# Optimization experiments

Measured on AMD Instinct MI355X. Metric: run time of the kernel, lower is better.

The kernel has to match this reference:

```python
import jax, jax.numpy as jnp
import numpy as np
import math

# ---- model dimensions (match init_kwargs / input_specs) ----
B, LQ, LK = 2, 1024, 1024          # batch, q_dim (query seq len), kv_dim (key seq len)
D_HEAD, H = 64, 16                 # head_size = d_model // n_heads, n_heads
D_MODEL = D_HEAD * H               # 1024
C_FACTOR = 5
U_SEL  = int(C_FACTOR * math.log(LQ))   # u  = 34 selected (top) queries
U_SAMP = int(LQ * math.log(LK))         # U  = 7097 randomly sampled keys


def setup_inputs() -> dict:
    key = jax.random.key(0)
    kq, kk, kv, kw, kb = jax.random.split(key, 5)
    q = jax.random.normal(kq, (B, LQ, D_HEAD), dtype=jnp.float32)
    k = jax.random.normal(kk, (B, LK, D_HEAD), dtype=jnp.float32)
    v = jax.random.normal(kv, (B, LK, D_HEAD), dtype=jnp.float32)
    # final projection Linear(n_heads*head_size, d_model), stored as (in, out)
    W_proj = jax.random.normal(kw, (D_MODEL, D_MODEL), dtype=jnp.float32) * 0.02
    b_proj = jax.random.normal(kb, (D_MODEL,), dtype=jnp.float32) * 0.02
    return {"q": q, "k": k, "v": v, "W_proj": W_proj, "b_proj": b_proj}


def _probsparse_head(head_key, q, k, v):
    """One ProbSparse head: q,k,v are (B, L, D_HEAD). Returns (B, LQ, D_HEAD)."""
    b_idx = jnp.arange(B)[:, None]
    # _sampler: per-batch random key indices, shape (B, U_SAMP)
    idx = jax.random.randint(head_key, (B, U_SAMP), 0, LK)
    k_bar = k[b_idx, idx]                                   # (B, U_SAMP, D)
    # sparsity measure M = max - mean over sampled scores
    s_bar = jnp.einsum('bqd,bud->bqu', q, k_bar)            # (B, LQ, U_SAMP)
    M = s_bar.max(axis=-1) - s_bar.mean(axis=-1)            # (B, LQ)
    _, top_idx = jax.lax.top_k(M, U_SEL)                    # (B, U_SEL)
    q_bar = q[b_idx, top_idx]                               # (B, U_SEL, D)
    # attention on the selected queries only; scale = sqrt(kv seq len) as in source
    attn = jnp.einsum('bud,bkd->buk', q_bar, k) / jnp.sqrt(jnp.float32(LK))
    attn = jax.nn.softmax(attn, axis=-1)
    s1 = jnp.einsum('buk,bkd->bud', attn, v)                # (B, U_SEL, D)
    # non-selected rows get mean(v); selected rows get attention output
    s = jnp.broadcast_to(v.mean(axis=1, keepdims=True), (B, LQ, D_HEAD))
    return s.at[b_idx, top_idx].set(s1)


def reference(q, k, v, W_proj, b_proj):
    # heads share q,k,v; differ only in random key sampling -> map sequentially over head keys
    head_keys = jax.random.split(jax.random.key(42), H)
    heads = jax.lax.map(lambda hk: _probsparse_head(hk, q, k, v), head_keys)  # (H,B,LQ,D)
    # concat along feature dim == transpose + reshape
    attn_out = jnp.transpose(heads, (1, 2, 0, 3)).reshape(B, LQ, H * D_HEAD)
    return attn_out @ W_proj + b_proj                        # (B, LQ, D_MODEL)
```

## Files before the change

kernel.cpp:

```cpp
#include <hip/hip_runtime.h>
#include <math.h>
#include <stdint.h>
#include <stddef.h>


#define BB     2
#define LQ     1024
#define LK     1024
#define DH     64
#define NH     16
#define DM     1024
#define USEL   34
#define USAMP  7097
#define NSLICE 8
#define NJ     8
#define JS     (LK / NJ)

#define THREEFRY_PARTITIONABLE 1

__device__ __forceinline__ uint32_t rotl32(uint32_t x, int d) {
  return (x << d) | (x >> (32 - d));
}

__device__ __forceinline__ void threefry2x32(uint32_t k0, uint32_t k1,
                                             uint32_t x0, uint32_t x1,
                                             uint32_t& o0, uint32_t& o1) {
  uint32_t ks2 = k0 ^ k1 ^ 0x1BD11BDAu;
  x0 += k0; x1 += k1;
#define TFR(r) { x0 += x1; x1 = rotl32(x1, (r)); x1 ^= x0; }
  TFR(13) TFR(15) TFR(26) TFR(6)
  x0 += k1; x1 += ks2 + 1u;
  TFR(17) TFR(29) TFR(16) TFR(24)
  x0 += ks2; x1 += k0 + 2u;
  TFR(13) TFR(15) TFR(26) TFR(6)
  x0 += k0; x1 += k1 + 3u;
  TFR(17) TFR(29) TFR(16) TFR(24)
  x0 += k1; x1 += ks2 + 4u;
  TFR(13) TFR(15) TFR(26) TFR(6)
  x0 += ks2; x1 += k0 + 5u;
#undef TFR
  o0 = x0; o1 = x1;
}

__global__ __launch_bounds__(1024) void k_sample(unsigned* __restrict__ counts) {
  int hb = blockIdx.x, h = hb >> 1, b = hb & 1;
  int t = threadIdx.x;
  __shared__ unsigned hist[LK];
  hist[t] = 0u;
  uint32_t sk0, sk1;
#if THREEFRY_PARTITIONABLE
  {
    uint32_t hk0, hk1;
    threefry2x32(0u, 42u, 0u, (uint32_t)h, hk0, hk1);
    threefry2x32(hk0, hk1, 0u, 1u, sk0, sk1);
  }
#else
  {
    uint32_t hk0, hk1, a0, a1, b0_, b1_, c0_, c1_;
    int i0 = 2 * h, i1 = 2 * h + 1;
    if (i0 < 16) { threefry2x32(0u, 42u, (uint32_t)i0, (uint32_t)(i0 + 16), a0, a1); hk0 = a0; }
    else         { threefry2x32(0u, 42u, (uint32_t)(i0 - 16), (uint32_t)i0, a0, a1); hk0 = a1; }
    if (i1 < 16) { threefry2x32(0u, 42u, (uint32_t)i1, (uint32_t)(i1 + 16), a0, a1); hk1 = a0; }
    else         { threefry2x32(0u, 42u, (uint32_t)(i1 - 16), (uint32_t)i1, a0, a1); hk1 = a1; }
    threefry2x32(hk0, hk1, 0u, 2u, b0_, b1_);
    threefry2x32(hk0, hk1, 1u, 3u, c0_, c1_);
    sk0 = b1_; sk1 = c1_;
  }
#endif
  __syncthreads();
  for (int j = t; j < USAMP; j += 1024) {
    uint32_t o0, o1, bits;
#if THREEFRY_PARTITIONABLE
    threefry2x32(sk0, sk1, 0u, (uint32_t)(b * USAMP + j), o0, o1);
    bits = o0 ^ o1;
#else
    threefry2x32(sk0, sk1, (uint32_t)j, (uint32_t)(j + USAMP), o0, o1);
    bits = (b == 0) ? o0 : o1;
#endif
    atomicAdd(&hist[bits & (LK - 1)], 1u);
  }
  __syncthreads();
  counts[(size_t)hb * LK + t] = hist[t];
}

__global__ __launch_bounds__(256) void k_means(const float* __restrict__ kk,
                                               const float* __restrict__ v,
                                               const unsigned* __restrict__ counts,
                                               float* __restrict__ kmean_part,
                                               float* __restrict__ vmean_part) {
  int task = blockIdx.y, s = blockIdx.x, t = threadIdx.x;
  int d4 = t & 15, jsub = t >> 4;
  __shared__ float4 part[16][16];
  float4 acc = make_float4(0.f, 0.f, 0.f, 0.f);
  if (task < NH * BB) {
    int b = task & 1;
    const unsigned* cnt = counts + (size_t)task * LK;
    const float4* kb4 = (const float4*)(kk + (size_t)b * LK * DH);
#pragma unroll
    for (int jj = 0; jj < LK / (16 * NSLICE); jj++) {
      int j = s * (LK / NSLICE) + jsub + 16 * jj;
      float c = (float)cnt[j];
      float4 kv = kb4[j * 16 + d4];
      acc.x += c * kv.x; acc.y += c * kv.y; acc.z += c * kv.z; acc.w += c * kv.w;
    }
  } else {
    int b = task - NH * BB;
    const float4* vb4 = (const float4*)(v + (size_t)b * LK * DH);
#pragma unroll
    for (int jj = 0; jj < LK / (16 * NSLICE); jj++) {
      int j = s * (LK / NSLICE) + jsub + 16 * jj;
      float4 kv = vb4[j * 16 + d4];
      acc.x += kv.x; acc.y += kv.y; acc.z += kv.z; acc.w += kv.w;
    }
  }
  part[jsub][d4] = acc;
  __syncthreads();
  if (t < 16) {
    float4 sum = part[0][t];
#pragma unroll
    for (int x = 1; x < 16; x++) {
      float4 p = part[x][t];
      sum.x += p.x; sum.y += p.y; sum.z += p.z; sum.w += p.w;
    }
    if (task < NH * BB) {
      float* dst = kmean_part + ((size_t)s * NH * BB + task) * DH;
      const float sc = 1.0f / (float)USAMP;
      dst[t * 4 + 0] = sum.x * sc; dst[t * 4 + 1] = sum.y * sc;
      dst[t * 4 + 2] = sum.z * sc; dst[t * 4 + 3] = sum.w * sc;
    } else {
      float* dst = vmean_part + ((size_t)s * BB + (task - NH * BB)) * DH;
      const float sc = 1.0f / (float)LK;
      dst[t * 4 + 0] = sum.x * sc; dst[t * 4 + 1] = sum.y * sc;
      dst[t * 4 + 2] = sum.z * sc; dst[t * 4 + 3] = sum.w * sc;
    }
  }
}

__global__ __launch_bounds__(256) void k_scores(const float* __restrict__ q,
                                                const float* __restrict__ k,
                                                float* __restrict__ S) {
  __shared__ float Qt[DH][68];
  __shared__ float Kt[DH][68];
  int b = blockIdx.z;
  int i0 = blockIdx.y * 64, j0 = blockIdx.x * 64;
  int t = threadIdx.x;
  const float* qb = q + ((size_t)b * LQ + i0) * DH;
  const float* kb = k + ((size_t)b * LK + j0) * DH;
#pragma unroll
  for (int rep = 0; rep < 4; rep++) {
    int lin = (rep * 256 + t) * 4;
    int r = lin >> 6, c = lin & 63;
    float4 qv = *(const float4*)(qb + (size_t)r * DH + c);
    float4 kv = *(const float4*)(kb + (size_t)r * DH + c);
    Qt[c][r] = qv.x; Qt[c + 1][r] = qv.y; Qt[c + 2][r] = qv.z; Qt[c + 3][r] = qv.w;
    Kt[c][r] = kv.x; Kt[c + 1][r] = kv.y; Kt[c + 2][r] = kv.z; Kt[c + 3][r] = kv.w;
  }
  __syncthreads();
  int tx = t & 15, ty = t >> 4;
  float acc[4][4] = {};
#pragma unroll 8
  for (int d = 0; d < DH; d++) {
    float4 av = *(const float4*)&Qt[d][ty * 4];
    float4 bv = *(const float4*)&Kt[d][tx * 4];
    acc[0][0] += av.x * bv.x; acc[0][1] += av.x * bv.y; acc[0][2] += av.x * bv.z; acc[0][3] += av.x * bv.w;
    acc[1][0] += av.y * bv.x; acc[1][1] += av.y * bv.y; acc[1][2] += av.y * bv.z; acc[1][3] += av.y * bv.w;
    acc[2][0] += av.z * bv.x; acc[2][1] += av.z * bv.y; acc[2][2] += av.z * bv.z; acc[2][3] += av.z * bv.w;
    acc[3][0] += av.w * bv.x; acc[3][1] += av.w * bv.y; acc[3][2] += av.w * bv.z; acc[3][3] += av.w * bv.w;
  }
  float* Sb = S + ((size_t)b * LQ + i0) * LK + j0;
#pragma unroll
  for (int r = 0; r < 4; r++) {
    *(float4*)(Sb + (size_t)(ty * 4 + r) * LK + tx * 4) =
        make_float4(acc[r][0], acc[r][1], acc[r][2], acc[r][3]);
  }
}

__global__ __launch_bounds__(256) void k_M(const float* __restrict__ q,
                                           const float* __restrict__ S,
                                           const unsigned* __restrict__ counts,
                                           const float* __restrict__ kmean_part,
                                           float* __restrict__ M) {
  int b = blockIdx.y;
  __shared__ uint32_t mask[NH][LK / 32];
  __shared__ float kmean_s[NH][DH];
  int t = threadIdx.x;
  for (int w = t; w < NH * (LK / 32); w += 256) {
    int h = w >> 5, blk = w & 31;
    const unsigned* cnt = counts + ((size_t)h * BB + b) * LK + blk * 32;
    uint32_t m = 0;
    for (int z = 0; z < 32; z++) m |= (cnt[z] != 0u ? 1u : 0u) << z;
    mask[h][blk] = m;
  }
  for (int idx = t; idx < NH * DH; idx += 256) {
    int h = idx >> 6, d = idx & 63;
    float sum = 0.f;
#pragma unroll
    for (int sl = 0; sl < NSLICE; sl++)
      sum += kmean_part[((size_t)sl * NH * BB + h * BB + b) * DH + d];
    kmean_s[h][d] = sum;
  }
  __syncthreads();
  int lane = t & 63, w4 = t >> 6;
  int i = blockIdx.x * 4 + w4;
  const float* Srow = S + ((size_t)b * LQ + i) * LK;
  float mx[NH];
#pragma unroll
  for (int h = 0; h < NH; h++) mx[h] = -INFINITY;
  for (int j = lane; j < LK; j += 64) {
    float s = Srow[j];
#pragma unroll
    for (int h = 0; h < NH; h++) {
      bool on = (mask[h][j >> 5] >> (j & 31)) & 1u;
      mx[h] = fmaxf(mx[h], on ? s : -INFINITY);
    }
  }
#pragma unroll
  for (int h = 0; h < NH; h++) {
#pragma unroll
    for (int off = 32; off > 0; off >>= 1) mx[h] = fmaxf(mx[h], __shfl_xor(mx[h], off));
  }
  float qv = q[((size_t)b * LQ + i) * DH + lane];
#pragma unroll
  for (int h = 0; h < NH; h++) {
    float p = qv * kmean_s[h][lane];
#pragma unroll
    for (int off = 32; off > 0; off >>= 1) p += __shfl_xor(p, off);
    mx[h] -= p;
  }
  if (lane == 0) {
#pragma unroll
    for (int h = 0; h < NH; h++) M[((size_t)h * BB + b) * LQ + i] = mx[h];
  }
}

__global__ __launch_bounds__(256) void k_topk(const float* __restrict__ M,
                                              int* __restrict__ topidx) {
  int hb = blockIdx.x, t = threadIdx.x;
  __shared__ float vals[LQ];
  __shared__ float wv[4];
  __shared__ int   wi[4];
  for (int i = t; i < LQ; i += 256) vals[i] = M[(size_t)hb * LQ + i];
  __syncthreads();
  int lane = t & 63, w = t >> 6;
  for (int u = 0; u < USEL; u++) {
    float bv = -INFINITY; int bi = 0x7fffffff;
#pragma unroll
    for (int r = 0; r < 4; r++) {
      int i = r * 256 + t;
      float x = vals[i];
      if (x > bv) { bv = x; bi = i; }
    }
#pragma unroll
    for (int off = 32; off > 0; off >>= 1) {
      float ov = __shfl_xor(bv, off);
      int   oi = __shfl_xor(bi, off);
      if (ov > bv || (ov == bv && oi < bi)) { bv = ov; bi = oi; }
    }
    if (lane == 0) { wv[w] = bv; wi[w] = bi; }
    __syncthreads();
    if (t == 0) {
      float fv = wv[0]; int fi = wi[0];
#pragma unroll
      for (int x = 1; x < 4; x++)
        if (wv[x] > fv || (wv[x] == fv && wi[x] < fi)) { fv = wv[x]; fi = wi[x]; }
      topidx[hb * USEL + u] = fi;
      vals[fi] = -INFINITY;
    }
    __syncthreads();
  }
}

__global__ __launch_bounds__(256) void k_pv(const float* __restrict__ S,
                                            const float* __restrict__ v,
                                            const int* __restrict__ topidx,
                                            float* __restrict__ delta_part,
                                            float* __restrict__ ssum_part) {
  int hb = blockIdx.y, s = blockIdx.x, b = hb & 1;
  int t = threadIdx.x, d = t & 63, g = t >> 6;
  __shared__ float p[USEL][JS];
  __shared__ float part[4][USEL][DH];
  for (int idx = t; idx < USEL * JS; idx += 256) {
    int u = idx >> 7, jj = idx & (JS - 1);
    int i = topidx[hb * USEL + u];
    float xs = S[((size_t)b * LQ + i) * LK + s * JS + jj];
    p[u][jj] = expf(xs * 0.03125f);
  }
  __syncthreads();
  float vreg[32];
  const float* vb = v + ((size_t)b * LK + s * JS + g * 32) * DH + d;
#pragma unroll
  for (int jj = 0; jj < 32; jj++) vreg[jj] = vb[(size_t)jj * DH];
  for (int u = 0; u < USEL; u++) {
    float acc = 0.f;
#pragma unroll
    for (int j4 = 0; j4 < 8; j4++) {
      float4 pp = *(const float4*)&p[u][g * 32 + j4 * 4];
      acc += pp.x * vreg[j4 * 4] + pp.y * vreg[j4 * 4 + 1] +
             pp.z * vreg[j4 * 4 + 2] + pp.w * vreg[j4 * 4 + 3];
    }
    part[g][u][d] = acc;
  }
  if (t < USEL * 4) {
    int u = t >> 2, ch = t & 3;
    float sum = 0.f;
#pragma unroll
    for (int jj = 0; jj < 32; jj++) sum += p[u][ch * 32 + jj];
    ssum_part[(((size_t)s * NH * BB + hb) * USEL + u) * 4 + ch] = sum;
  }
  __syncthreads();
  for (int idx = t; idx < USEL * DH; idx += 256) {
    int u = idx >> 6, dd = idx & 63;
    float sum = part[0][u][dd] + part[1][u][dd] + part[2][u][dd] + part[3][u][dd];
    delta_part[(((size_t)s * NH * BB + hb) * USEL + u) * DH + dd] = sum;
  }
}

__global__ __launch_bounds__(256) void k_base(const float* __restrict__ W,
                                              const float* __restrict__ vmean_part,
                                              float* __restrict__ base_part) {
  __shared__ float vm[DH];
  int b = blockIdx.y, hc = blockIdx.z;
  int o = blockIdx.x * 256 + threadIdx.x;
  if (threadIdx.x < DH) {
    float s = 0.f;
#pragma unroll
    for (int sl = 0; sl < NSLICE; sl++)
      s += vmean_part[((size_t)sl * BB + b) * DH + threadIdx.x];
    vm[threadIdx.x] = s;
  }
  __syncthreads();
  const float* Wr = W + (size_t)hc * DH * DM + o;
  float acc = 0.f;
#pragma unroll
  for (int d = 0; d < DH; d++) acc += vm[d] * Wr[(size_t)d * DM];
  base_part[((size_t)hc * BB + b) * DM + o] = acc;
}

__global__ __launch_bounds__(256) void k_fill(const float* __restrict__ base_part,
                                              const float* __restrict__ bproj,
                                              float* __restrict__ out) {
  int idx = blockIdx.x * 256 + threadIdx.x;
  int o4 = idx & (DM / 4 - 1);
  int b = (idx >> 18) & 1;
  float4 bs = ((const float4*)bproj)[o4];
#pragma unroll
  for (int hc = 0; hc < NH; hc++) {
    float4 p = ((const float4*)base_part)[((size_t)hc * BB + b) * (DM / 4) + o4];
    bs.x += p.x; bs.y += p.y; bs.z += p.z; bs.w += p.w;
  }
  ((float4*)out)[idx] = bs;
}

__global__ __launch_bounds__(256) void k_corr(const float* __restrict__ W,
                                              const int* __restrict__ topidx,
                                              const float* __restrict__ delta_part,
                                              const float* __restrict__ ssum_part,
                                              const float* __restrict__ vmean_part,
                                              float* __restrict__ out) {
  int u = blockIdx.x, hb = blockIdx.y;
  int h = hb >> 1, b = hb & 1;
  int t = threadIdx.x;
  __shared__ float dl[DH];
  int i = topidx[hb * USEL + u];
  if (t < DH) {
    float ss = 0.f, dr = 0.f, vm = 0.f;
#pragma unroll
    for (int sl = 0; sl < NJ; sl++) {
      const float* sp = ssum_part + (((size_t)sl * NH * BB + hb) * USEL + u) * 4;
      ss += sp[0] + sp[1] + sp[2] + sp[3];
      dr += delta_part[(((size_t)sl * NH * BB + hb) * USEL + u) * DH + t];
    }
#pragma unroll
    for (int sl = 0; sl < NSLICE; sl++)
      vm += vmean_part[((size_t)sl * BB + b) * DH + t];
    dl[t] = dr / ss - vm;
  }
  __syncthreads();
  const float* Wh = W + (size_t)h * DH * DM;
  float* orow = out + ((size_t)b * LQ + i) * DM;
#pragma unroll
  for (int rep = 0; rep < 4; rep++) {
    int o = rep * 256 + t;
    float acc = 0.f;
#pragma unroll 16
    for (int d = 0; d < DH; d++) acc += dl[d] * Wh[(size_t)d * DM + o];
    atomicAdd(&orow[o], acc);
  }
}

extern "C" void kernel_launch(void* const* d_in, const int* in_sizes, int n_in,
                              void* d_out, int out_size, void* d_ws, size_t ws_size,
                              hipStream_t stream) {
  const float* q  = (const float*)d_in[0];
  const float* k  = (const float*)d_in[1];
  const float* v  = (const float*)d_in[2];
  const float* W  = (const float*)d_in[3];
  const float* bp = (const float*)d_in[4];
  float* out = (float*)d_out;

  float* S = out;

  char* w = (char*)d_ws;
  unsigned* counts     = (unsigned*)w;  w += (size_t)NH * BB * LK * 4;
  float*    kmean_part = (float*)w;     w += (size_t)NSLICE * NH * BB * DH * 4;
  float*    vmean_part = (float*)w;     w += (size_t)NSLICE * BB * DH * 4;
  float*    base_part  = (float*)w;     w += (size_t)NH * BB * DM * 4;
  float*    delta_part = (float*)w;     w += (size_t)NJ * NH * BB * USEL * DH * 4;
  float*    ssum_part  = (float*)w;     w += (size_t)NJ * NH * BB * USEL * 4 * 4;
  float*    M          = (float*)w;     w += (size_t)NH * BB * LQ * 4;
  int*      topidx     = (int*)w;       w += (size_t)NH * BB * USEL * 4;
  if ((size_t)(w - (char*)d_ws) > ws_size) return;

  k_sample<<<NH * BB, 1024, 0, stream>>>(counts);
  k_means <<<dim3(NSLICE, NH * BB + BB), 256, 0, stream>>>(k, v, counts, kmean_part, vmean_part);
  k_scores<<<dim3(LK / 64, LQ / 64, BB), 256, 0, stream>>>(q, k, S);
  k_M     <<<dim3(LQ / 4, BB), 256, 0, stream>>>(q, S, counts, kmean_part, M);
  k_topk  <<<NH * BB, 256, 0, stream>>>(M, topidx);
  k_pv    <<<dim3(NJ, NH * BB), 256, 0, stream>>>(S, v, topidx, delta_part, ssum_part);
  k_base  <<<dim3(DM / 256, BB, NH), 256, 0, stream>>>(W, vmean_part, base_part);
  k_fill  <<<(BB * LQ * DM / 4) / 256, 256, 0, stream>>>(base_part, bp, out);
  k_corr  <<<dim3(USEL, NH * BB), 256, 0, stream>>>(W, topidx, delta_part, ssum_part, vmean_part, out);
}
```

Baseline: 178.2 us.

## Merge independent kernels into heterogeneous launches and move scores buffer to workspace

Combines the sampling, mean, and score kernels into one launch with block-index dispatch, fuses the M computation with the base projection, and fuses top-k with the output fill, cutting nine launches to five. Sampling now builds the key bitmask and full key means in one block per head, so the partial-slice reductions disappear. The score matrix moves from the output buffer to workspace, which the fused fill requires because it now runs before k_pv reads S. The trade-off is uneven block workloads within each launch, and the 32 sampling blocks do serial work while the GEMM blocks run.

```diff
diff --git a/kernel.cpp b/kernel.cpp
--- a/kernel.cpp
+++ b/kernel.cpp
@@ -12,9 +12,11 @@
 #define DM     1024
 #define USEL   34
 #define USAMP  7097
-#define NSLICE 8
 #define NJ     8
 #define JS     (LK / NJ)
+#define NSC    512
+#define NMB    512
+#define NTK    32
 
 #define THREEFRY_PARTITIONABLE 1
 
@@ -42,231 +44,266 @@
   o0 = x0; o1 = x1;
 }
 
-__global__ __launch_bounds__(1024) void k_sample(unsigned* __restrict__ counts) {
-  int hb = blockIdx.x, h = hb >> 1, b = hb & 1;
-  int t = threadIdx.x;
-  __shared__ unsigned hist[LK];
-  hist[t] = 0u;
-  uint32_t sk0, sk1;
+__device__ __forceinline__ void randint_key(int h, uint32_t& sk0, uint32_t& sk1) {
 #if THREEFRY_PARTITIONABLE
-  {
-    uint32_t hk0, hk1;
-    threefry2x32(0u, 42u, 0u, (uint32_t)h, hk0, hk1);
-    threefry2x32(hk0, hk1, 0u, 1u, sk0, sk1);
-  }
+  uint32_t hk0, hk1;
+  threefry2x32(0u, 42u, 0u, (uint32_t)h, hk0, hk1);
+  threefry2x32(hk0, hk1, 0u, 1u, sk0, sk1);
 #else
-  {
-    uint32_t hk0, hk1, a0, a1, b0_, b1_, c0_, c1_;
-    int i0 = 2 * h, i1 = 2 * h + 1;
-    if (i0 < 16) { threefry2x32(0u, 42u, (uint32_t)i0, (uint32_t)(i0 + 16), a0, a1); hk0 = a0; }
-    else         { threefry2x32(0u, 42u, (uint32_t)(i0 - 16), (uint32_t)i0, a0, a1); hk0 = a1; }
-    if (i1 < 16) { threefry2x32(0u, 42u, (uint32_t)i1, (uint32_t)(i1 + 16), a0, a1); hk1 = a0; }
-    else         { threefry2x32(0u, 42u, (uint32_t)(i1 - 16), (uint32_t)i1, a0, a1); hk1 = a1; }
-    threefry2x32(hk0, hk1, 0u, 2u, b0_, b1_);
-    threefry2x32(hk0, hk1, 1u, 3u, c0_, c1_);
-    sk0 = b1_; sk1 = c1_;
-  }
+  uint32_t hk0, hk1, a0, a1, b0_, b1_, c0_, c1_;
+  int i0 = 2 * h, i1 = 2 * h + 1;
+  if (i0 < 16) { threefry2x32(0u, 42u, (uint32_t)i0, (uint32_t)(i0 + 16), a0, a1); hk0 = a0; }
+  else         { threefry2x32(0u, 42u, (uint32_t)(i0 - 16), (uint32_t)i0, a0, a1); hk0 = a1; }
+  if (i1 < 16) { threefry2x32(0u, 42u, (uint32_t)i1, (uint32_t)(i1 + 16), a0, a1); hk1 = a0; }
+  else         { threefry2x32(0u, 42u, (uint32_t)(i1 - 16), (uint32_t)i1, a0, a1); hk1 = a1; }
+  threefry2x32(hk0, hk1, 0u, 2u, b0_, b1_);
+  threefry2x32(hk0, hk1, 1u, 3u, c0_, c1_);
+  sk0 = b1_; sk1 = c1_;
 #endif
-  __syncthreads();
-  for (int j = t; j < USAMP; j += 1024) {
-    uint32_t o0, o1, bits;
+}
+
+__global__ __launch_bounds__(256) void k_prep_scores(const float* __restrict__ q,
+                                                     const float* __restrict__ kk,
+                                                     const float* __restrict__ v,
+                                                     float* __restrict__ S,
+                                                     unsigned* __restrict__ mask_g,
+                                                     float* __restrict__ kmean,
+                                                     float* __restrict__ vmean) {
+  __shared__ __align__(16) char smem[34816];
+  int bx = blockIdx.x, t = threadIdx.x;
+  if (bx < NSC) {
+    float (*Qt)[68] = (float (*)[68])smem;
+    float (*Kt)[68] = (float (*)[68])(smem + 17408);
+    int b = bx >> 8, it = (bx >> 4) & 15, jt = bx & 15;
+    int i0 = it * 64, j0 = jt * 64;
+    const float* qb = q + ((size_t)b * LQ + i0) * DH;
+    const float* kb = kk + ((size_t)b * LK + j0) * DH;
+#pragma unroll
+    for (int rep = 0; rep < 4; rep++) {
+      int lin = (rep * 256 + t) * 4;
+      int r = lin >> 6, c = lin & 63;
+      float4 qv = *(const float4*)(qb + (size_t)r * DH + c);
+      float4 kv = *(const float4*)(kb + (size_t)r * DH + c);
+      Qt[c][r] = qv.x; Qt[c + 1][r] = qv.y; Qt[c + 2][r] = qv.z; Qt[c + 3][r] = qv.w;
+      Kt[c][r] = kv.x; Kt[c + 1][r] = kv.y; Kt[c + 2][r] = kv.z; Kt[c + 3][r] = kv.w;
+    }
+    __syncthreads();
+    int tx = t & 15, ty = t >> 4;
+    float acc[4][4] = {};
+#pragma unroll 8
+    for (int d = 0; d < DH; d++) {
+      float4 av = *(const float4*)&Qt[d][ty * 4];
+      float4 bv = *(const float4*)&Kt[d][tx * 4];
+      acc[0][0] += av.x * bv.x; acc[0][1] += av.x * bv.y; acc[0][2] += av.x * bv.z; acc[0][3] += av.x * bv.w;
+      acc[1][0] += av.y * bv.x; acc[1][1] += av.y * bv.y; acc[1][2] += av.y * bv.z; acc[1][3] += av.y * bv.w;
+      acc[2][0] += av.z * bv.x; acc[2][1] += av.z * bv.y; acc[2][2] += av.z * bv.z; acc[2][3] += av.z * bv.w;
+      acc[3][0] += av.w * bv.x; acc[3][1] += av.w * bv.y; acc[3][2] += av.w * bv.z; acc[3][3] += av.w * bv.w;
+    }
+    float* Sb = S + ((size_t)b * LQ + i0) * LK + j0;
+#pragma unroll
+    for (int r = 0; r < 4; r++) {
+      *(float4*)(Sb + (size_t)(ty * 4 + r) * LK + tx * 4) =
+          make_float4(acc[r][0], acc[r][1], acc[r][2], acc[r][3]);
+    }
+  } else if (bx < NSC + NH * BB) {
+    int hb = bx - NSC, h = hb >> 1, b = hb & 1;
+    unsigned* hist = (unsigned*)smem;
+    float4 (*part)[16] = (float4 (*)[16])(smem + 4096);
+    hist[t] = 0u; hist[t + 256] = 0u; hist[t + 512] = 0u; hist[t + 768] = 0u;
+    uint32_t sk0, sk1;
+    randint_key(h, sk0, sk1);
+    __syncthreads();
+    for (int j = t; j < USAMP; j += 256) {
+      uint32_t o0, o1, bits;
 #if THREEFRY_PARTITIONABLE
-    threefry2x32(sk0, sk1, 0u, (uint32_t)(b * USAMP + j), o0, o1);
-    bits = o0 ^ o1;
+      threefry2x32(sk0, sk1, 0u, (uint32_t)(b * USAMP + j), o0, o1);
+      bits = o0 ^ o1;
 #else
-    threefry2x32(sk0, sk1, (uint32_t)j, (uint32_t)(j + USAMP), o0, o1);
-    bits = (b == 0) ? o0 : o1;
+      threefry2x32(sk0, sk1, (uint32_t)j, (uint32_t)(j + USAMP), o0, o1);
+      bits = (b == 0) ? o0 : o1;
 #endif
-    atomicAdd(&hist[bits & (LK - 1)], 1u);
-  }
-  __syncthreads();
-  counts[(size_t)hb * LK + t] = hist[t];
-}
-
-__global__ __launch_bounds__(256) void k_means(const float* __restrict__ kk,
-                                               const float* __restrict__ v,
-                                               const unsigned* __restrict__ counts,
-                                               float* __restrict__ kmean_part,
-                                               float* __restrict__ vmean_part) {
-  int task = blockIdx.y, s = blockIdx.x, t = threadIdx.x;
-  int d4 = t & 15, jsub = t >> 4;
-  __shared__ float4 part[16][16];
-  float4 acc = make_float4(0.f, 0.f, 0.f, 0.f);
-  if (task < NH * BB) {
-    int b = task & 1;
-    const unsigned* cnt = counts + (size_t)task * LK;
+      atomicAdd(&hist[bits & (LK - 1)], 1u);
+    }
+    __syncthreads();
+    if (t < LK / 32) {
+      uint32_t m = 0;
+      for (int z = 0; z < 32; z++) m |= (hist[t * 32 + z] != 0u ? 1u : 0u) << z;
+      mask_g[hb * (LK / 32) + t] = m;
+    }
+    int d4 = t & 15, jsub = t >> 4;
     const float4* kb4 = (const float4*)(kk + (size_t)b * LK * DH);
-#pragma unroll
-    for (int jj = 0; jj < LK / (16 * NSLICE); jj++) {
-      int j = s * (LK / NSLICE) + jsub + 16 * jj;
-      float c = (float)cnt[j];
+    float4 acc = make_float4(0.f, 0.f, 0.f, 0.f);
+#pragma unroll 8
+    for (int jj = 0; jj < LK / 16; jj++) {
+      int j = jsub + 16 * jj;
+      float c = (float)hist[j];
       float4 kv = kb4[j * 16 + d4];
       acc.x += c * kv.x; acc.y += c * kv.y; acc.z += c * kv.z; acc.w += c * kv.w;
     }
+    part[jsub][d4] = acc;
+    __syncthreads();
+    if (t < 16) {
+      float4 sum = part[0][t];
+#pragma unroll
+      for (int x = 1; x < 16; x++) {
+        float4 p = part[x][t];
+        sum.x += p.x; sum.y += p.y; sum.z += p.z; sum.w += p.w;
+      }
+      const float sc = 1.0f / (float)USAMP;
+      float* dst = kmean + (size_t)hb * DH;
+      dst[t * 4 + 0] = sum.x * sc; dst[t * 4 + 1] = sum.y * sc;
+      dst[t * 4 + 2] = sum.z * sc; dst[t * 4 + 3] = sum.w * sc;
+    }
   } else {
-    int b = task - NH * BB;
+    int b = bx - NSC - NH * BB;
+    float4 (*part)[16] = (float4 (*)[16])smem;
+    int d4 = t & 15, jsub = t >> 4;
     const float4* vb4 = (const float4*)(v + (size_t)b * LK * DH);
-#pragma unroll
-    for (int jj = 0; jj < LK / (16 * NSLICE); jj++) {
-      int j = s * (LK / NSLICE) + jsub + 16 * jj;
+    float4 acc = make_float4(0.f, 0.f, 0.f, 0.f);
+#pragma unroll 8
+    for (int jj = 0; jj < LK / 16; jj++) {
+      int j = jsub + 16 * jj;
       float4 kv = vb4[j * 16 + d4];
       acc.x += kv.x; acc.y += kv.y; acc.z += kv.z; acc.w += kv.w;
     }
-  }
-  part[jsub][d4] = acc;
-  __syncthreads();
-  if (t < 16) {
-    float4 sum = part[0][t];
-#pragma unroll
-    for (int x = 1; x < 16; x++) {
-      float4 p = part[x][t];
-      sum.x += p.x; sum.y += p.y; sum.z += p.z; sum.w += p.w;
-    }
-    if (task < NH * BB) {
-      float* dst = kmean_part + ((size_t)s * NH * BB + task) * DH;
-      const float sc = 1.0f / (float)USAMP;
+    part[jsub][d4] = acc;
+    __syncthreads();
+    if (t < 16) {
+      float4 sum = part[0][t];
+#pragma unroll
+      for (int x = 1; x < 16; x++) {
+        float4 p = part[x][t];
+        sum.x += p.x; sum.y += p.y; sum.z += p.z; sum.w += p.w;
+      }
+      const float sc = 1.0f / (float)LK;
+      float* dst = vmean + (size_t)b * DH;
       dst[t * 4 + 0] = sum.x * sc; dst[t * 4 + 1] = sum.y * sc;
       dst[t * 4 + 2] = sum.z * sc; dst[t * 4 + 3] = sum.w * sc;
-    } else {
-      float* dst = vmean_part + ((size_t)s * BB + (task - NH * BB)) * DH;
-      const float sc = 1.0f / (float)LK;
-      dst[t * 4 + 0] = sum.x * sc; dst[t * 4 + 1] = sum.y * sc;
-      dst[t * 4 + 2] = sum.z * sc; dst[t * 4 + 3] = sum.w * sc;
-    }
-  }
-}
-
-__global__ __launch_bounds__(256) void k_scores(const float* __restrict__ q,
-                                                const float* __restrict__ k,
-                                                float* __restrict__ S) {
-  __shared__ float Qt[DH][68];
-  __shared__ float Kt[DH][68];
-  int b = blockIdx.z;
-  int i0 = blockIdx.y * 64, j0 = blockIdx.x * 64;
-  int t = threadIdx.x;
-  const float* qb = q + ((size_t)b * LQ + i0) * DH;
-  const float* kb = k + ((size_t)b * LK + j0) * DH;
-#pragma unroll
-  for (int rep = 0; rep < 4; rep++) {
-    int lin = (rep * 256 + t) * 4;
-    int r = lin >> 6, c = lin & 63;
-    float4 qv = *(const float4*)(qb + (size_t)r * DH + c);
-    float4 kv = *(const float4*)(kb + (size_t)r * DH + c);
-    Qt[c][r] = qv.x; Qt[c + 1][r] = qv.y; Qt[c + 2][r] = qv.z; Qt[c + 3][r] = qv.w;
-    Kt[c][r] = kv.x; Kt[c + 1][r] = kv.y; Kt[c + 2][r] = kv.z; Kt[c + 3][r] = kv.w;
-  }
-  __syncthreads();
-  int tx = t & 15, ty = t >> 4;
-  float acc[4][4] = {};
-#pragma unroll 8
-  for (int d = 0; d < DH; d++) {
-    float4 av = *(const float4*)&Qt[d][ty * 4];
-    float4 bv = *(const float4*)&Kt[d][tx * 4];
-    acc[0][0] += av.x * bv.x; acc[0][1] += av.x * bv.y; acc[0][2] += av.x * bv.z; acc[0][3] += av.x * bv.w;
-    acc[1][0] += av.y * bv.x; acc[1][1] += av.y * bv.y; acc[1][2] += av.y * bv.z; acc[1][3] += av.y * bv.w;
-    acc[2][0] += av.z * bv.x; acc[2][1] += av.z * bv.y; acc[2][2] += av.z * bv.z; acc[2][3] += av.z * bv.w;
-    acc[3][0] += av.w * bv.x; acc[3][1] += av.w * bv.y; acc[3][2] += av.w * bv.z; acc[3][3] += av.w * bv.w;
-  }
-  float* Sb = S + ((size_t)b * LQ + i0) * LK + j0;
-#pragma unroll
-  for (int r = 0; r < 4; r++) {
-    *(float4*)(Sb + (size_t)(ty * 4 + r) * LK + tx * 4) =
-        make_float4(acc[r][0], acc[r][1], acc[r][2], acc[r][3]);
-  }
-}
-
-__global__ __launch_bounds__(256) void k_M(const float* __restrict__ q,
-                                           const float* __restrict__ S,
-                                           const unsigned* __restrict__ counts,
-                                           const float* __restrict__ kmean_part,
-                                           float* __restrict__ M) {
-  int b = blockIdx.y;
-  __shared__ uint32_t mask[NH][LK / 32];
-  __shared__ float kmean_s[NH][DH];
-  int t = threadIdx.x;
-  for (int w = t; w < NH * (LK / 32); w += 256) {
-    int h = w >> 5, blk = w & 31;
-    const unsigned* cnt = counts + ((size_t)h * BB + b) * LK + blk * 32;
-    uint32_t m = 0;
-    for (int z = 0; z < 32; z++) m |= (cnt[z] != 0u ? 1u : 0u) << z;
-    mask[h][blk] = m;
-  }
-  for (int idx = t; idx < NH * DH; idx += 256) {
-    int h = idx >> 6, d = idx & 63;
-    float sum = 0.f;
-#pragma unroll
-    for (int sl = 0; sl < NSLICE; sl++)
-      sum += kmean_part[((size_t)sl * NH * BB + h * BB + b) * DH + d];
-    kmean_s[h][d] = sum;
-  }
-  __syncthreads();
-  int lane = t & 63, w4 = t >> 6;
-  int i = blockIdx.x * 4 + w4;
-  const float* Srow = S + ((size_t)b * LQ + i) * LK;
-  float mx[NH];
-#pragma unroll
-  for (int h = 0; h < NH; h++) mx[h] = -INFINITY;
-  for (int j = lane; j < LK; j += 64) {
-    float s = Srow[j];
+    }
+  }
+}
+
+__global__ __launch_bounds__(256) void k_M_base(const float* __restrict__ q,
+                                                const float* __restrict__ S,
+                                                const unsigned* __restrict__ mask_g,
+                                                const float* __restrict__ kmean,
+                                                const float* __restrict__ vmean,
+                                                const float* __restrict__ W,
+                                                float* __restrict__ M,
+                                                float* __restrict__ base_part) {
+  __shared__ __align__(16) char smem[6400];
+  int bx = blockIdx.x, t = threadIdx.x;
+  if (bx < NMB) {
+    int b = bx >> 8, iblk = bx & 255;
+    uint32_t (*mask)[LK / 32] = (uint32_t (*)[LK / 32])smem;
+    float (*kmean_s)[DH] = (float (*)[DH])(smem + 2048);
+    for (int w = t; w < NH * (LK / 32); w += 256) {
+      int h = w >> 5, blk = w & 31;
+      mask[h][blk] = mask_g[(size_t)(h * BB + b) * (LK / 32) + blk];
+    }
+    for (int idx = t; idx < NH * DH; idx += 256) {
+      int h = idx >> 6, d = idx & 63;
+      kmean_s[h][d] = kmean[(size_t)(h * BB + b) * DH + d];
+    }
+    __syncthreads();
+    int lane = t & 63, w4 = t >> 6;
+    int i = iblk * 4 + w4;
+    const float* Srow = S + ((size_t)b * LQ + i) * LK;
+    float mx[NH];
+#pragma unroll
+    for (int h = 0; h < NH; h++) mx[h] = -INFINITY;
+    for (int j = lane; j < LK; j += 64) {
+      float s = Srow[j];
+#pragma unroll
+      for (int h = 0; h < NH; h++) {
+        bool on = (mask[h][j >> 5] >> (j & 31)) & 1u;
+        mx[h] = fmaxf(mx[h], on ? s : -INFINITY);
+      }
+    }
 #pragma unroll
     for (int h = 0; h < NH; h++) {
-      bool on = (mask[h][j >> 5] >> (j & 31)) & 1u;
-      mx[h] = fmaxf(mx[h], on ? s : -INFINITY);
-    }
-  }
-#pragma unroll
-  for (int h = 0; h < NH; h++) {
-#pragma unroll
-    for (int off = 32; off > 0; off >>= 1) mx[h] = fmaxf(mx[h], __shfl_xor(mx[h], off));
-  }
-  float qv = q[((size_t)b * LQ + i) * DH + lane];
-#pragma unroll
-  for (int h = 0; h < NH; h++) {
-    float p = qv * kmean_s[h][lane];
-#pragma unroll
-    for (int off = 32; off > 0; off >>= 1) p += __shfl_xor(p, off);
-    mx[h] -= p;
-  }
-  if (lane == 0) {
-#pragma unroll
-    for (int h = 0; h < NH; h++) M[((size_t)h * BB + b) * LQ + i] = mx[h];
-  }
-}
-
-__global__ __launch_bounds__(256) void k_topk(const float* __restrict__ M,
-                                              int* __restrict__ topidx) {
-  int hb = blockIdx.x, t = threadIdx.x;
-  __shared__ float vals[LQ];
-  __shared__ float wv[4];
-  __shared__ int   wi[4];
-  for (int i = t; i < LQ; i += 256) vals[i] = M[(size_t)hb * LQ + i];
-  __syncthreads();
-  int lane = t & 63, w = t >> 6;
-  for (int u = 0; u < USEL; u++) {
-    float bv = -INFINITY; int bi = 0x7fffffff;
-#pragma unroll
-    for (int r = 0; r < 4; r++) {
-      int i = r * 256 + t;
-      float x = vals[i];
-      if (x > bv) { bv = x; bi = i; }
-    }
-#pragma unroll
-    for (int off = 32; off > 0; off >>= 1) {
-      float ov = __shfl_xor(bv, off);
-      int   oi = __shfl_xor(bi, off);
-      if (ov > bv || (ov == bv && oi < bi)) { bv = ov; bi = oi; }
-    }
-    if (lane == 0) { wv[w] = bv; wi[w] = bi; }
-    __syncthreads();
-    if (t == 0) {
-      float fv = wv[0]; int fi = wi[0];
-#pragma unroll
-      for (int x = 1; x < 4; x++)
-        if (wv[x] > fv || (wv[x] == fv && wi[x] < fi)) { fv = wv[x]; fi = wi[x]; }
-      topidx[hb * USEL + u] = fi;
-      vals[fi] = -INFINITY;
-    }
-    __syncthreads();
+#pragma unroll
+      for (int off = 32; off > 0; off >>= 1) mx[h] = fmaxf(mx[h], __shfl_xor(mx[h], off));
+    }
+    float qv = q[((size_t)b * LQ + i) * DH + lane];
+#pragma unroll
+    for (int h = 0; h < NH; h++) {
+      float p = qv * kmean_s[h][lane];
+#pragma unroll
+      for (int off = 32; off > 0; off >>= 1) p += __shfl_xor(p, off);
+      mx[h] -= p;
+    }
+    if (lane == 0) {
+#pragma unroll
+      for (int h = 0; h < NH; h++) M[((size_t)h * BB + b) * LQ + i] = mx[h];
+    }
+  } else {
+    int idx = bx - NMB;
+    int ob = idx & 3, b = (idx >> 2) & 1, hc = idx >> 3;
+    float* vm = (float*)smem;
+    if (t < DH) vm[t] = vmean[b * DH + t];
+    __syncthreads();
+    int o = ob * 256 + t;
+    const float* Wr = W + (size_t)hc * DH * DM + o;
+    float acc = 0.f;
+#pragma unroll
+    for (int d = 0; d < DH; d++) acc += vm[d] * Wr[(size_t)d * DM];
+    base_part[((size_t)hc * BB + b) * DM + o] = acc;
+  }
+}
+
+__global__ __launch_bounds__(256) void k_topk_fill(const float* __restrict__ M,
+                                                   int* __restrict__ topidx,
+                                                   const float* __restrict__ base_part,
+                                                   const float* __restrict__ bproj,
+                                                   float* __restrict__ out) {
+  __shared__ __align__(16) char smem[4160];
+  int bx = blockIdx.x, t = threadIdx.x;
+  if (bx < NTK) {
+    int hb = bx;
+    float* vals = (float*)smem;
+    float* wv = (float*)(smem + 4096);
+    int* wi = (int*)(smem + 4112);
+    for (int i = t; i < LQ; i += 256) vals[i] = M[(size_t)hb * LQ + i];
+    __syncthreads();
+    int lane = t & 63, w = t >> 6;
+    for (int u = 0; u < USEL; u++) {
+      float bv = -INFINITY; int bi = 0x7fffffff;
+#pragma unroll
+      for (int r = 0; r < 4; r++) {
+        int i = r * 256 + t;
+        float x = vals[i];
+        if (x > bv) { bv = x; bi = i; }
+      }
+#pragma unroll
+      for (int off = 32; off > 0; off >>= 1) {
+        float ov = __shfl_xor(bv, off);
+        int   oi = __shfl_xor(bi, off);
+        if (ov > bv || (ov == bv && oi < bi)) { bv = ov; bi = oi; }
+      }
+      if (lane == 0) { wv[w] = bv; wi[w] = bi; }
+      __syncthreads();
+      if (t == 0) {
+        float fv = wv[0]; int fi = wi[0];
+#pragma unroll
+        for (int x = 1; x < 4; x++)
+          if (wv[x] > fv || (wv[x] == fv && wi[x] < fi)) { fv = wv[x]; fi = wi[x]; }
+        topidx[hb * USEL + u] = fi;
+        vals[fi] = -INFINITY;
+      }
+      __syncthreads();
+    }
+  } else {
+    int idx = (bx - NTK) * 256 + t;
+    int o4 = idx & (DM / 4 - 1);
+    int b = (idx >> 18) & 1;
+    float4 bs = ((const float4*)bproj)[o4];
+#pragma unroll
+    for (int hc = 0; hc < NH; hc++) {
+      float4 p = ((const float4*)base_part)[((size_t)hc * BB + b) * (DM / 4) + o4];
+      bs.x += p.x; bs.y += p.y; bs.z += p.z; bs.w += p.w;
+    }
+    ((float4*)out)[idx] = bs;
   }
 }
 
@@ -315,47 +352,11 @@
   }
 }
 
-__global__ __launch_bounds__(256) void k_base(const float* __restrict__ W,
-                                              const float* __restrict__ vmean_part,
-                                              float* __restrict__ base_part) {
-  __shared__ float vm[DH];
-  int b = blockIdx.y, hc = blockIdx.z;
-  int o = blockIdx.x * 256 + threadIdx.x;
-  if (threadIdx.x < DH) {
-    float s = 0.f;
-#pragma unroll
-    for (int sl = 0; sl < NSLICE; sl++)
-      s += vmean_part[((size_t)sl * BB + b) * DH + threadIdx.x];
-    vm[threadIdx.x] = s;
-  }
-  __syncthreads();
-  const float* Wr = W + (size_t)hc * DH * DM + o;
-  float acc = 0.f;
-#pragma unroll
-  for (int d = 0; d < DH; d++) acc += vm[d] * Wr[(size_t)d * DM];
-  base_part[((size_t)hc * BB + b) * DM + o] = acc;
-}
-
-__global__ __launch_bounds__(256) void k_fill(const float* __restrict__ base_part,
-                                              const float* __restrict__ bproj,
-                                              float* __restrict__ out) {
-  int idx = blockIdx.x * 256 + threadIdx.x;
-  int o4 = idx & (DM / 4 - 1);
-  int b = (idx >> 18) & 1;
-  float4 bs = ((const float4*)bproj)[o4];
-#pragma unroll
-  for (int hc = 0; hc < NH; hc++) {
-    float4 p = ((const float4*)base_part)[((size_t)hc * BB + b) * (DM / 4) + o4];
-    bs.x += p.x; bs.y += p.y; bs.z += p.z; bs.w += p.w;
-  }
-  ((float4*)out)[idx] = bs;
-}
-
 __global__ __launch_bounds__(256) void k_corr(const float* __restrict__ W,
                                               const int* __restrict__ topidx,
                                               const float* __restrict__ delta_part,
                                               const float* __restrict__ ssum_part,
-                                              const float* __restrict__ vmean_part,
+                                              const float* __restrict__ vmean,
                                               float* __restrict__ out) {
   int u = blockIdx.x, hb = blockIdx.y;
   int h = hb >> 1, b = hb & 1;
@@ -363,17 +364,14 @@
   __shared__ float dl[DH];
   int i = topidx[hb * USEL + u];
   if (t < DH) {
-    float ss = 0.f, dr = 0.f, vm = 0.f;
+    float ss = 0.f, dr = 0.f;
 #pragma unroll
     for (int sl = 0; sl < NJ; sl++) {
       const float* sp = ssum_part + (((size_t)sl * NH * BB + hb) * USEL + u) * 4;
       ss += sp[0] + sp[1] + sp[2] + sp[3];
       dr += delta_part[(((size_t)sl * NH * BB + hb) * USEL + u) * DH + t];
     }
-#pragma unroll
-    for (int sl = 0; sl < NSLICE; sl++)
-      vm += vmean_part[((size_t)sl * BB + b) * DH + t];
-    dl[t] = dr / ss - vm;
+    dl[t] = dr / ss - vmean[b * DH + t];
   }
   __syncthreads();
   const float* Wh = W + (size_t)h * DH * DM;
@@ -398,12 +396,11 @@
   const float* bp = (const float*)d_in[4];
   float* out = (float*)d_out;
 
-  float* S = out;
-
   char* w = (char*)d_ws;
-  unsigned* counts     = (unsigned*)w;  w += (size_t)NH * BB * LK * 4;
-  float*    kmean_part = (float*)w;     w += (size_t)NSLICE * NH * BB * DH * 4;
-  float*    vmean_part = (float*)w;     w += (size_t)NSLICE * BB * DH * 4;
+  float*    S          = (float*)w;     w += (size_t)BB * LQ * LK * 4;
+  unsigned* mask_g     = (unsigned*)w;  w += (size_t)NH * BB * (LK / 32) * 4;
+  float*    kmean      = (float*)w;     w += (size_t)NH * BB * DH * 4;
+  float*    vmean      = (float*)w;     w += (size_t)BB * DH * 4;
   float*    base_part  = (float*)w;     w += (size_t)NH * BB * DM * 4;
   float*    delta_part = (float*)w;     w += (size_t)NJ * NH * BB * USEL * DH * 4;
   float*    ssum_part  = (float*)w;     w += (size_t)NJ * NH * BB * USEL * 4 * 4;
@@ -411,13 +408,9 @@
   int*      topidx     = (int*)w;       w += (size_t)NH * BB * USEL * 4;
   if ((size_t)(w - (char*)d_ws) > ws_size) return;
 
-  k_sample<<<NH * BB, 1024, 0, stream>>>(counts);
-  k_means <<<dim3(NSLICE, NH * BB + BB), 256, 0, stream>>>(k, v, counts, kmean_part, vmean_part);
-  k_scores<<<dim3(LK / 64, LQ / 64, BB), 256, 0, stream>>>(q, k, S);
-  k_M     <<<dim3(LQ / 4, BB), 256, 0, stream>>>(q, S, counts, kmean_part, M);
-  k_topk  <<<NH * BB, 256, 0, stream>>>(M, topidx);
-  k_pv    <<<dim3(NJ, NH * BB), 256, 0, stream>>>(S, v, topidx, delta_part, ssum_part);
-  k_base  <<<dim3(DM / 256, BB, NH), 256, 0, stream>>>(W, vmean_part, base_part);
-  k_fill  <<<(BB * LQ * DM / 4) / 256, 256, 0, stream>>>(base_part, bp, out);
-  k_corr  <<<dim3(USEL, NH * BB), 256, 0, stream>>>(W, topidx, delta_part, ssum_part, vmean_part, out);
-}
+  k_prep_scores<<<NSC + NH * BB + BB, 256, 0, stream>>>(q, k, v, S, mask_g, kmean, vmean);
+  k_M_base     <<<NMB + NH * BB * (DM / 256), 256, 0, stream>>>(q, S, mask_g, kmean, vmean, W, M, base_part);
+  k_topk_fill  <<<NTK + (BB * LQ * DM / 4) / 256, 256, 0, stream>>>(M, topidx, base_part, bp, out);
+  k_pv         <<<dim3(NJ, NH * BB), 256, 0, stream>>>(S, v, topidx, delta_part, ssum_part);
+  k_corr       <<<dim3(USEL, NH * BB), 256, 0, stream>>>(W, topidx, delta_part, ssum_part, vmean, out);
+}
```

New measurement: 158.1 us. 1.13x faster.
